# Optimization experiments

Hardware: AMD Instinct MI355X
Metric: run time of the kernel (lower is better)

The kernel has to match this reference:

```python
import jax, jax.numpy as jnp
from jax import lax
import numpy as np
import math

B, T, D = 4, 4096, 1024
K, H = 128, 8
KH = K // H
KER = 4
M = 4 * D  # mlp hidden


def _ln(x, g, b):
    m = jnp.mean(x, axis=-1, keepdims=True)
    v = jnp.var(x, axis=-1, keepdims=True)
    return (x - m) / jnp.sqrt(v + 1e-5) * g + b


def setup_inputs() -> dict:
    key = jax.random.key(0)
    ks = jax.random.split(key, 20)
    s = lambda i, shape, sc=0.02: jax.random.normal(ks[i], shape, dtype=jnp.float32) * sc
    inp = {}
    inp["x"] = jax.random.normal(ks[0], (B, T, D), dtype=jnp.float32)
    inp["prev_eig"] = jax.random.normal(ks[1], (B, T, 2 * K), dtype=jnp.float32)
    inp["in_proj_w"] = s(2, (2 * K, D))
    inp["conv_w"] = s(3, (2 * K, 1, KER), 0.3)          # depthwise Conv1d weight
    inp["conv_b"] = s(4, (2 * K,), 0.02)
    inp["mem_gate"] = jnp.float32(-3.0)
    inp["mem_proj_w"] = jnp.eye(2 * K, dtype=jnp.float32) + s(5, (2 * K, 2 * K), 0.02)
    # log_decay uniform in [center-1, center+0.5], center = -2 + 1.5*(1/5)
    center = -2.0 + 1.5 * (1.0 / 5.0)
    inp["log_decay"] = jax.random.uniform(ks[6], (K,), dtype=jnp.float32, minval=center - 1.0, maxval=center + 0.5)
    inp["frequency"] = jnp.linspace(0.0, 2.0 * math.pi * (1.0 - 1.0 / K), K, dtype=jnp.float32)
    inp["coupling"] = jnp.eye(KH, dtype=jnp.float32)[None] + 0.01 * jax.random.normal(ks[7], (H, KH, KH), dtype=jnp.float32) / math.sqrt(KH)
    inp["out_proj_w"] = s(8, (D, 2 * K))
    inp["gate_w"] = s(9, (D, D))
    inp["gate_b"] = jnp.full((D,), -2.0, dtype=jnp.float32)
    inp["mlp_w1"] = s(10, (M, D))
    inp["mlp_b1"] = jnp.zeros((M,), jnp.float32)
    inp["mlp_w2"] = s(11, (D, M))
    inp["mlp_b2"] = jnp.zeros((D,), jnp.float32)
    inp["n1_g"] = jnp.ones((D,), jnp.float32)
    inp["n1_b"] = jnp.zeros((D,), jnp.float32)
    inp["n2_g"] = jnp.ones((D,), jnp.float32)
    inp["n2_b"] = jnp.zeros((D,), jnp.float32)
    return inp


def reference(x, prev_eig, in_proj_w, conv_w, conv_b, mem_gate, mem_proj_w,
              log_decay, frequency, coupling, out_proj_w, gate_w, gate_b,
              mlp_w1, mlp_b1, mlp_w2, mlp_b2, n1_g, n1_b, n2_g, n2_b):
    Bn, Tn, Dn = x.shape
    xn = _ln(x, n1_g, n1_b)
    beta = xn @ in_proj_w.T                                   # [B,T,2K]
    # depthwise causal conv: torch pad=ker-1 both sides then [:, :, :T] == left-pad ker-1 + valid
    ker = conv_w.shape[-1]
    bp = jnp.pad(beta, ((0, 0), (ker - 1, 0), (0, 0))).transpose(0, 2, 1)  # [B,2K,T+ker-1]
    beta = lax.conv_general_dilated(bp, conv_w, (1,), 'VALID',
                                    feature_group_count=conv_w.shape[0],
                                    dimension_numbers=('NCH', 'OIH', 'NCH'))
    beta = jax.nn.silu(beta.transpose(0, 2, 1) + conv_b)       # [B,T,2K]
    br, bi = jnp.split(beta, 2, axis=-1)                       # [B,T,K] each
    # memory injection (has_memory: layer_idx > 0)
    mg = jax.nn.sigmoid(mem_gate)
    pr, pi = jnp.split(prev_eig @ mem_proj_w.T, 2, axis=-1)
    br = br + mg * pr
    bi = bi + mg * pi
    # eigenstate evolution via zero-padded complex FFT convolution
    mag = jax.nn.sigmoid(log_decay)                            # [K]
    n = jnp.arange(Tn, dtype=x.dtype)
    mag_pow = mag[None, :] ** n[:, None]                       # [T,K]
    phase = n[:, None] * frequency[None, :]
    kern = mag_pow * (jnp.cos(phase) + 1j * jnp.sin(phase))    # complex [T,K]
    beta_c = br + 1j * bi
    Bf = jnp.fft.fft(jnp.pad(beta_c, ((0, 0), (0, Tn), (0, 0))), axis=1)  # [B,2T,K]
    Kf = jnp.fft.fft(jnp.pad(kern, ((0, Tn), (0, 0))), axis=0)            # [2T,K]
    c = jnp.fft.ifft(Bf * Kf[None], axis=1)[:, :Tn]
    cr, ci = c.real.astype(x.dtype), c.imag.astype(x.dtype)
    # per-head coupling, batched over heads
    Hh, Kh = coupling.shape[0], coupling.shape[1]
    cr = jnp.einsum('hjk,bthk->bthj', coupling, cr.reshape(Bn, Tn, Hh, Kh)).reshape(Bn, Tn, Hh * Kh)
    ci = jnp.einsum('hjk,bthk->bthj', coupling, ci.reshape(Bn, Tn, Hh, Kh)).reshape(Bn, Tn, Hh * Kh)
    eig = jnp.concatenate([cr, ci], axis=-1)                   # [B,T,2K]
    h = jax.nn.sigmoid(xn @ gate_w.T + gate_b) * (eig @ out_proj_w.T)
    x1 = x + h
    y = _ln(x1, n2_g, n2_b)
    x2 = x1 + jax.nn.silu(y @ mlp_w1.T + mlp_b1) @ mlp_w2.T + mlp_b2
    return (x2, eig)
```

## Files before the change

kernel.cpp:

```cpp
#include <hip/hip_runtime.h>
#include <hip/hip_bf16.h>
#include <math.h>

#define Bn 4
#define Tn 4096
#define Dn 1024
#define Kn 128
#define TWOK 256
#define Hn 8
#define Mmlp 4096
#define NROW (Bn * Tn)
#define TAPS 16

typedef __attribute__((ext_vector_type(8))) short bf16x8;
typedef __attribute__((ext_vector_type(4))) float floatx4;

__device__ __forceinline__ float sigmoidf_(float x) { return 1.f / (1.f + __expf(-x)); }

__global__ __launch_bounds__(256) void f2bf_kernel(const float* __restrict__ in,
                                                   __hip_bfloat16* __restrict__ out,
                                                   int n) {
    const int i = (blockIdx.x * 256 + threadIdx.x) * 4;
    if (i >= n) return;
    const float4 v = *(const float4*)(in + i);
    out[i + 0] = __float2bfloat16(v.x);
    out[i + 1] = __float2bfloat16(v.y);
    out[i + 2] = __float2bfloat16(v.z);
    out[i + 3] = __float2bfloat16(v.w);
}

__global__ __launch_bounds__(256) void ln_kernel(const float* __restrict__ x,
                                                 const float* __restrict__ g,
                                                 const float* __restrict__ b,
                                                 __hip_bfloat16* __restrict__ out) {
    const int row = blockIdx.x;
    const float4* xr = (const float4*)(x + (size_t)row * Dn);
    float4 v = xr[threadIdx.x];
    float s = v.x + v.y + v.z + v.w;
    float ss = v.x * v.x + v.y * v.y + v.z * v.z + v.w * v.w;
    for (int off = 32; off; off >>= 1) {
        s += __shfl_down(s, off);
        ss += __shfl_down(ss, off);
    }
    __shared__ float rs[4], rss[4];
    const int wv = threadIdx.x >> 6, ln = threadIdx.x & 63;
    if (ln == 0) { rs[wv] = s; rss[wv] = ss; }
    __syncthreads();
    s = rs[0] + rs[1] + rs[2] + rs[3];
    ss = rss[0] + rss[1] + rss[2] + rss[3];
    const float mean = s * (1.f / Dn);
    const float var = ss * (1.f / Dn) - mean * mean;
    const float inv = rsqrtf(var + 1e-5f);
    const float4 gg = ((const float4*)g)[threadIdx.x];
    const float4 bb = ((const float4*)b)[threadIdx.x];
    __hip_bfloat16* op = out + (size_t)row * Dn + threadIdx.x * 4;
    op[0] = __float2bfloat16((v.x - mean) * inv * gg.x + bb.x);
    op[1] = __float2bfloat16((v.y - mean) * inv * gg.y + bb.y);
    op[2] = __float2bfloat16((v.z - mean) * inv * gg.z + bb.z);
    op[3] = __float2bfloat16((v.w - mean) * inv * gg.w + bb.w);
}

template <int EPI, typename CT>
__global__ __launch_bounds__(256, 4)
void gemm_bf(const ushort* __restrict__ A,
             const ushort* __restrict__ B,
             CT* __restrict__ C,
             int M, int N, int Kd,
             const float* __restrict__ bias) {
    __shared__ ushort As[128 * 32];
    __shared__ ushort Bs[128 * 32];
    const int tid = threadIdx.x;
    const int nbx = gridDim.x;
    const int nblk = nbx * gridDim.y;
    int bid = blockIdx.y * nbx + blockIdx.x;
    if ((nblk & 7) == 0)
        bid = (bid & 7) * (nblk >> 3) + (bid >> 3);
    const int m0 = (bid / nbx) * 128, n0 = (bid % nbx) * 128;
    const int wave = tid >> 6, lane = tid & 63;
    const int wm = wave >> 1, wn = wave & 1;
    const int mlane = lane & 15, quad = lane >> 4;

    floatx4 acc[4][4] = {};

    {
        const ushort* Ap = A + (size_t)m0 * Kd;
        const ushort* Bp = B + (size_t)n0 * Kd;
        for (int k0 = 0; k0 < Kd; k0 += 32) {
#pragma unroll
            for (int q = 0; q < 2; ++q) {
                const int c = q * 256 + tid;
                const int row = c >> 2, kc = (c & 3) * 8;
                __builtin_amdgcn_global_load_lds(
                    (const __attribute__((address_space(1))) void*)(Ap + (size_t)row * Kd + k0 + kc),
                    (__attribute__((address_space(3))) void*)(As + c * 8), 16, 0, 0);
                __builtin_amdgcn_global_load_lds(
                    (const __attribute__((address_space(1))) void*)(Bp + (size_t)row * Kd + k0 + kc),
                    (__attribute__((address_space(3))) void*)(Bs + c * 8), 16, 0, 0);
            }
            __syncthreads();
            bf16x8 af[4], bfr[4];
#pragma unroll
            for (int t = 0; t < 4; ++t) {
                af[t]  = *(const bf16x8*)&As[(wm * 64 + t * 16 + mlane) * 32 + quad * 8];
                bfr[t] = *(const bf16x8*)&Bs[(wn * 64 + t * 16 + mlane) * 32 + quad * 8];
            }
#pragma unroll
            for (int i = 0; i < 4; ++i)
#pragma unroll
                for (int j = 0; j < 4; ++j)
                    acc[i][j] = __builtin_amdgcn_mfma_f32_16x16x32_bf16(af[i], bfr[j], acc[i][j], 0, 0, 0);
            __syncthreads();
        }
    }

    float s_pre = 0.f;
    if constexpr (EPI == 1) s_pre = sigmoidf_(bias[0]);

    const int cbase = n0 + wn * 64 + mlane;
#pragma unroll
    for (int i = 0; i < 4; ++i) {
#pragma unroll
        for (int r = 0; r < 4; ++r) {
            const int row = m0 + wm * 64 + i * 16 + quad * 4 + r;
            const size_t ro = (size_t)row * N;
#pragma unroll
            for (int j = 0; j < 4; ++j) {
                const int col = cbase + j * 16;
                const float a = acc[i][j][r];
                float o;
                if constexpr (EPI == 0) o = a;
                else                    o = s_pre * a;
                if constexpr (__is_same(CT, float)) C[ro + col] = o;
                else                                C[ro + col] = __float2bfloat16(o);
            }
        }
    }
}

template <int EPI, typename CT>
__global__ __launch_bounds__(512, 2)
void gemmP(const ushort* __restrict__ A, const ushort* __restrict__ B,
           CT* __restrict__ C, int N, int Kd,
           const float* __restrict__ bias, const float* __restrict__ aux1,
           const __hip_bfloat16* __restrict__ aux2, int cg) {
    __shared__ ushort As[4 * 8192];
    __shared__ ushort Bs[4 * 8192];
    const int tid = threadIdx.x;
    const int nbx = gridDim.x;
    const int nblk = nbx * gridDim.y;
    const int nrows = nblk / nbx;
    int bid = blockIdx.y * nbx + blockIdx.x;
    int mt, ntile;
    if ((nblk & 7) == 0 && cg > 0 && nbx % cg == 0 && nrows % (8 / cg) == 0) {
        const int xcd = bid & 7, i = bid >> 3;
        const int cPerG = nbx / cg;
        const int rPerG = nrows / (8 / cg);
        const int rg = xcd / cg, cgi = xcd % cg;
        mt = rg * rPerG + i / cPerG;
        ntile = cgi * cPerG + i % cPerG;
    } else {
        mt = bid / nbx; ntile = bid % nbx;
    }
    const int m0 = mt * 256, n0 = ntile * 256;
    const int wave = tid >> 6, lane = tid & 63;
    const int wm = wave >> 2, wn = wave & 3;
    const int mlane = lane & 15, quad = lane >> 4;
    const int oswz = (quad ^ ((mlane >> 1) & 3)) * 8;
    const int NT = Kd >> 5;

    const int cA0 = tid, cA1 = 512 + tid;
    const int rA0 = cA0 >> 2, rA1 = cA1 >> 2;
    const ushort* aSrc0 = A + (size_t)(m0 + rA0) * Kd + (((cA0 & 3) ^ ((rA0 >> 1) & 3)) << 3);
    const ushort* aSrc1 = A + (size_t)(m0 + rA1) * Kd + (((cA1 & 3) ^ ((rA1 >> 1) & 3)) << 3);
    const ushort* bSrc0 = B + (size_t)(n0 + rA0) * Kd + (((cA0 & 3) ^ ((rA0 >> 1) & 3)) << 3);
    const ushort* bSrc1 = B + (size_t)(n0 + rA1) * Kd + (((cA1 & 3) ^ ((rA1 >> 1) & 3)) << 3);

    auto stage = [&](int t) {
        const int s = (t & 3) * 8192;
        const int kk = t << 5;
        __builtin_amdgcn_global_load_lds(
            (const __attribute__((address_space(1))) void*)(aSrc0 + kk),
            (__attribute__((address_space(3))) void*)(As + s + cA0 * 8), 16, 0, 0);
        __builtin_amdgcn_global_load_lds(
            (const __attribute__((address_space(1))) void*)(aSrc1 + kk),
            (__attribute__((address_space(3))) void*)(As + s + cA1 * 8), 16, 0, 0);
        __builtin_amdgcn_global_load_lds(
            (const __attribute__((address_space(1))) void*)(bSrc0 + kk),
            (__attribute__((address_space(3))) void*)(Bs + s + cA0 * 8), 16, 0, 0);
        __builtin_amdgcn_global_load_lds(
            (const __attribute__((address_space(1))) void*)(bSrc1 + kk),
            (__attribute__((address_space(3))) void*)(Bs + s + cA1 * 8), 16, 0, 0);
    };

    floatx4 acc[8][4] = {};
    bf16x8 fa0[8], fb0[4], fa1[8], fb1[4];

    const int arow = wm * 128 + mlane;
    const int brow = wn * 64 + mlane;

#define RDSET(FA, FB, T)                                                     \
    {                                                                        \
        const ushort* lA = As + ((T) & 3) * 8192;                            \
        const ushort* lB = Bs + ((T) & 3) * 8192;                            \
        _Pragma("unroll")                                                    \
        for (int f_ = 0; f_ < 8; ++f_)                                       \
            FA[f_] = *(const bf16x8*)(lA + (arow + f_ * 16) * 32 + oswz);    \
        _Pragma("unroll")                                                    \
        for (int g_ = 0; g_ < 4; ++g_)                                       \
            FB[g_] = *(const bf16x8*)(lB + (brow + g_ * 16) * 32 + oswz);    \
    }

#define MMSET(FA, FB)                                                        \
    __builtin_amdgcn_s_setprio(1);                                           \
    _Pragma("unroll")                                                        \
    for (int f_ = 0; f_ < 8; ++f_) {                                         \
        _Pragma("unroll")                                                    \
        for (int g_ = 0; g_ < 4; ++g_) {                                     \
            acc[f_][g_] = __builtin_amdgcn_mfma_f32_16x16x32_bf16(           \
                FA[f_], FB[g_], acc[f_][g_], 0, 0, 0);                       \
        }                                                                    \
    }                                                                        \
    __builtin_amdgcn_s_setprio(0);

#define VMW(T)                                                               \
    if ((T) + 1 < NT) { asm volatile("s_waitcnt vmcnt(4)" ::: "memory"); }   \
    else              { asm volatile("s_waitcnt vmcnt(0)" ::: "memory"); }

    stage(0); stage(1);
    VMW(0)
    __builtin_amdgcn_s_barrier();
    RDSET(fa0, fb0, 0)
    if (2 < NT) stage(2);
    VMW(1)
    __builtin_amdgcn_s_barrier();
    RDSET(fa1, fb1, 1)
    if (3 < NT) stage(3);
    MMSET(fa0, fb0)
    for (int u = 1; u < (NT >> 1); ++u) {
        const int te = 2 * u;
        VMW(te)
        __builtin_amdgcn_s_barrier();
        RDSET(fa0, fb0, te)
        if (te + 2 < NT) stage(te + 2);
        MMSET(fa1, fb1)
        const int to = te + 1;
        VMW(to)
        __builtin_amdgcn_s_barrier();
        RDSET(fa1, fb1, to)
        if (to + 2 < NT) stage(to + 2);
        MMSET(fa0, fb0)
    }
    MMSET(fa1, fb1)
#undef RDSET
#undef MMSET
#undef VMW

    const int cbase = n0 + wn * 64 + mlane;
#pragma unroll
    for (int f = 0; f < 8; ++f) {
#pragma unroll
        for (int r = 0; r < 4; ++r) {
            const int row = m0 + wm * 128 + f * 16 + quad * 4 + r;
            const size_t ro = (size_t)row * N;
#pragma unroll
            for (int g = 0; g < 4; ++g) {
                const int col = cbase + g * 16;
                const float av = acc[f][g][r];
                float o;
                if constexpr (EPI == 0) {
                    o = av;
                } else if constexpr (EPI == 2) {
                    o = aux1[ro + col] + sigmoidf_(av + bias[col]) * __bfloat162float(aux2[ro + col]);
                } else if constexpr (EPI == 3) {
                    const float tt = av + bias[col];
                    o = tt * sigmoidf_(tt);
                } else {
                    o = av + bias[col] + aux1[ro + col];
                }
                if constexpr (__is_same(CT, float)) C[ro + col] = o;
                else                                C[ro + col] = __float2bfloat16(o);
            }
        }
    }
}

#define TCH 256
#define BROWS (TCH + TAPS + 2)
#define UROWS (TCH + TAPS - 1)

__global__ __launch_bounds__(256) void cfc_kernel(const float* __restrict__ beta,
                                                  const float* __restrict__ mgp,
                                                  const float* __restrict__ conv_w,
                                                  const float* __restrict__ conv_b,
                                                  const float* __restrict__ log_decay,
                                                  const float* __restrict__ freq,
                                                  const float* __restrict__ coup,
                                                  float* __restrict__ eig,
                                                  __hip_bfloat16* __restrict__ eig_bf) {
    const int b = blockIdx.z, h = blockIdx.y, t0 = blockIdx.x * TCH;
    const int tid = threadIdx.x;

    __shared__ float sbeta[BROWS * 32];
    __shared__ float su[UROWS * 33];
    __shared__ float str[16 * TAPS], sti[16 * TAPS];
    __shared__ float scoup[16 * 16];
    __shared__ float scw[32 * 4], scb[32];

    auto chan = [&](int cg) { return (cg < 16) ? (h * 16 + cg) : (128 + h * 16 + cg - 16); };

    for (int idx = tid; idx < BROWS * 32; idx += 256) {
        const int r = idx >> 5, cg = idx & 31;
        const int t = t0 - (TAPS + 2) + r;
        sbeta[idx] = (t >= 0) ? beta[((size_t)b * Tn + t) * TWOK + chan(cg)] : 0.f;
    }
    for (int idx = tid; idx < UROWS * 32; idx += 256) {
        const int r = idx >> 5, cg = idx & 31;
        const int t = t0 - (TAPS - 1) + r;
        su[r * 33 + cg] = (t >= 0) ? mgp[((size_t)b * Tn + t) * TWOK + chan(cg)] : 0.f;
    }
    if (tid < 128) scw[tid] = conv_w[chan(tid >> 2) * 4 + (tid & 3)];
    else if (tid < 160) scb[tid - 128] = conv_b[chan(tid - 128)];
    scoup[tid] = coup[h * 256 + tid];
    {
        const int k = tid >> 4, d = tid & (TAPS - 1);
        const float mag = sigmoidf_(log_decay[h * 16 + k]);
        const float f = freq[h * 16 + k];
        const float p = powf(mag, (float)d);
        str[k * TAPS + d] = p * cosf(d * f);
        sti[k * TAPS + d] = p * sinf(d * f);
    }
    __syncthreads();

    for (int idx = tid; idx < UROWS * 32; idx += 256) {
        const int r = idx >> 5, cg = idx & 31;
        const int rb = r + 3;
        float v = sbeta[(rb - 3) * 32 + cg] * scw[cg * 4 + 0] +
                  sbeta[(rb - 2) * 32 + cg] * scw[cg * 4 + 1] +
                  sbeta[(rb - 1) * 32 + cg] * scw[cg * 4 + 2] +
                  sbeta[(rb - 0) * 32 + cg] * scw[cg * 4 + 3] + scb[cg];
        v = v * sigmoidf_(v);
        su[r * 33 + cg] += v;
    }
    __syncthreads();

    const int ru = tid + (TAPS - 1);
    float orr[16], oii[16];
#pragma unroll
    for (int j = 0; j < 16; ++j) { orr[j] = 0.f; oii[j] = 0.f; }
#pragma unroll 4
    for (int k = 0; k < 16; ++k) {
        float accr = 0.f, acci = 0.f;
#pragma unroll
        for (int d = 0; d < TAPS; ++d) {
            const float ur = su[(ru - d) * 33 + k];
            const float ui = su[(ru - d) * 33 + 16 + k];
            const float lr = str[k * TAPS + d], li = sti[k * TAPS + d];
            accr += lr * ur - li * ui;
            acci += lr * ui + li * ur;
        }
#pragma unroll
        for (int j = 0; j < 16; ++j) {
            orr[j] += scoup[j * 16 + k] * accr;
            oii[j] += scoup[j * 16 + k] * acci;
        }
    }
    const size_t base = ((size_t)b * Tn + t0 + tid) * TWOK + h * 16;
    float4* er = (float4*)(eig + base);
    float4* ei = (float4*)(eig + base + Kn);
#pragma unroll
    for (int q = 0; q < 4; ++q) {
        er[q] = make_float4(orr[4 * q], orr[4 * q + 1], orr[4 * q + 2], orr[4 * q + 3]);
        ei[q] = make_float4(oii[4 * q], oii[4 * q + 1], oii[4 * q + 2], oii[4 * q + 3]);
    }
#pragma unroll
    for (int j = 0; j < 16; ++j) {
        eig_bf[base + j] = __float2bfloat16(orr[j]);
        eig_bf[base + Kn + j] = __float2bfloat16(oii[j]);
    }
}

extern "C" void kernel_launch(void* const* d_in, const int* in_sizes, int n_in,
                              void* d_out, int out_size, void* d_ws, size_t ws_size,
                              hipStream_t stream) {
    const float* x          = (const float*)d_in[0];
    const float* prev_eig   = (const float*)d_in[1];
    const float* in_proj_w  = (const float*)d_in[2];
    const float* conv_w     = (const float*)d_in[3];
    const float* conv_b     = (const float*)d_in[4];
    const float* mem_gate   = (const float*)d_in[5];
    const float* mem_proj_w = (const float*)d_in[6];
    const float* log_decay  = (const float*)d_in[7];
    const float* frequency  = (const float*)d_in[8];
    const float* coupling   = (const float*)d_in[9];
    const float* out_proj_w = (const float*)d_in[10];
    const float* gate_w     = (const float*)d_in[11];
    const float* gate_b     = (const float*)d_in[12];
    const float* mlp_w1     = (const float*)d_in[13];
    const float* mlp_b1     = (const float*)d_in[14];
    const float* mlp_w2     = (const float*)d_in[15];
    const float* mlp_b2     = (const float*)d_in[16];
    const float* n1_g       = (const float*)d_in[17];
    const float* n1_b       = (const float*)d_in[18];
    const float* n2_g       = (const float*)d_in[19];
    const float* n2_b       = (const float*)d_in[20];

    float* out = (float*)d_out;
    float* eig = out + (size_t)NROW * Dn;

    char* wsb = (char*)d_ws;
    const size_t MB = 1 << 20;
    const bool bigws = ws_size >= 252 * MB;

    float* x1    = (float*)(wsb + 0);
    float* beta  = (float*)(wsb + 0);
    float* mgp   = (float*)(wsb + 16 * MB);
    __hip_bfloat16 *h1, *eig_bf, *peig_bf, *xn_bf, *y_bf, *w1_bf, *w2_bf,
                   *gate_bf, *inpj_bf, *outpj_bf, *mempj_bf;
    if (bigws) {
        h1       = (__hip_bfloat16*)(wsb + 64 * MB);
        xn_bf    = (__hip_bfloat16*)(wsb + 192 * MB);
        y_bf     = (__hip_bfloat16*)(wsb + 192 * MB);
        w1_bf    = (__hip_bfloat16*)(wsb + 224 * MB);
        w2_bf    = (__hip_bfloat16*)(wsb + 232 * MB);
        gate_bf  = (__hip_bfloat16*)(wsb + 240 * MB);
        inpj_bf  = (__hip_bfloat16*)(wsb + 242 * MB);
        outpj_bf = (__hip_bfloat16*)(wsb + 242 * MB + 512 * 1024);
        mempj_bf = (__hip_bfloat16*)(wsb + 243 * MB);
        peig_bf  = (__hip_bfloat16*)(wsb + 244 * MB);
        eig_bf   = (__hip_bfloat16*)(wsb + 244 * MB);
    } else {
        h1       = (__hip_bfloat16*)(wsb + 64 * MB);
        eig_bf   = (__hip_bfloat16*)(wsb + 96 * MB);
        peig_bf  = (__hip_bfloat16*)(wsb + 104 * MB);
        xn_bf    = (__hip_bfloat16*)(wsb + 128 * MB);
        y_bf     = (__hip_bfloat16*)(wsb + 160 * MB);
        w1_bf    = (__hip_bfloat16*)(wsb + 192 * MB);
        w2_bf    = (__hip_bfloat16*)(wsb + 200 * MB);
        gate_bf  = (__hip_bfloat16*)(wsb + 208 * MB);
        inpj_bf  = (__hip_bfloat16*)(wsb + 210 * MB);
        outpj_bf = (__hip_bfloat16*)(wsb + 210 * MB + 512 * 1024);
        mempj_bf = (__hip_bfloat16*)(wsb + 211 * MB);
    }

    auto cvt = [&](const float* src, __hip_bfloat16* dst, int n) {
        f2bf_kernel<<<dim3((n / 4 + 255) / 256), dim3(256), 0, stream>>>(src, dst, n);
    };
    cvt(in_proj_w,  inpj_bf,  TWOK * Dn);
    cvt(mem_proj_w, mempj_bf, TWOK * TWOK);
    cvt(out_proj_w, outpj_bf, Dn * TWOK);
    cvt(gate_w,     gate_bf,  Dn * Dn);
    cvt(mlp_w1,     w1_bf,    Mmlp * Dn);
    cvt(mlp_w2,     w2_bf,    Dn * Mmlp);
    cvt(prev_eig,   peig_bf,  NROW * TWOK);

    ln_kernel<<<dim3(NROW), dim3(256), 0, stream>>>(x, n1_g, n1_b, xn_bf);
    gemm_bf<0, float><<<dim3(2, 128), dim3(256), 0, stream>>>(
        (const ushort*)xn_bf, (const ushort*)inpj_bf, beta, NROW, TWOK, Dn, nullptr);
    gemm_bf<1, float><<<dim3(2, 128), dim3(256), 0, stream>>>(
        (const ushort*)peig_bf, (const ushort*)mempj_bf, mgp, NROW, TWOK, TWOK, mem_gate);
    cfc_kernel<<<dim3(Tn / TCH, Hn, Bn), dim3(256), 0, stream>>>(
        beta, mgp, conv_w, conv_b, log_decay, frequency, coupling, eig, eig_bf);
    gemmP<0, __hip_bfloat16><<<dim3(4, 64), dim3(512), 0, stream>>>(
        (const ushort*)eig_bf, (const ushort*)outpj_bf, h1, Dn, TWOK,
        nullptr, nullptr, nullptr, 2);
    gemmP<2, float><<<dim3(4, 64), dim3(512), 0, stream>>>(
        (const ushort*)xn_bf, (const ushort*)gate_bf, x1, Dn, Dn,
        gate_b, x, h1, 2);
    ln_kernel<<<dim3(NROW), dim3(256), 0, stream>>>(x1, n2_g, n2_b, y_bf);
    if (bigws) {
        gemmP<3, __hip_bfloat16><<<dim3(16, 64), dim3(512), 0, stream>>>(
            (const ushort*)y_bf, (const ushort*)w1_bf, h1, Mmlp, Dn,
            mlp_b1, nullptr, nullptr, 2);
        gemmP<4, float><<<dim3(4, 64), dim3(512), 0, stream>>>(
            (const ushort*)h1, (const ushort*)w2_bf, out, Dn, Mmlp,
            mlp_b2, x1, nullptr, 2);
    } else {
        for (int ck = 0; ck < 2; ++ck) {
            const size_t roff = (size_t)ck * 8192 * Dn;
            gemmP<3, __hip_bfloat16><<<dim3(16, 32), dim3(512), 0, stream>>>(
                (const ushort*)(y_bf + roff), (const ushort*)w1_bf, h1, Mmlp, Dn,
                mlp_b1, nullptr, nullptr, 2);
            gemmP<4, float><<<dim3(8, 32), dim3(512), 0, stream>>>(
                (const ushort*)h1, (const ushort*)w2_bf, out + roff, Dn, Mmlp,
                mlp_b2, x1 + roff, nullptr, 2);
        }
    }
}
```

Before: 706.4 us.

## Merge weight/input bf16 conversions into one launch and change gemmP last argument

Replaces seven separate fp32-to-bf16 conversion launches with a single grid-stride kernel that walks a concatenated index range and dispatches to the right source/destination pair. This is meant to cut launch overhead and tail effects from the small conversions. The final integer argument of several gemmP launches also changes from 2 to 1. Its meaning is not visible, but it likely selects a different scheduling or split mode for the narrow-output GEMMs.

```diff
diff --git a/kernel.cpp b/kernel.cpp
--- a/kernel.cpp
+++ b/kernel.cpp
@@ -17,16 +17,30 @@
 
 __device__ __forceinline__ float sigmoidf_(float x) { return 1.f / (1.f + __expf(-x)); }
 
-__global__ __launch_bounds__(256) void f2bf_kernel(const float* __restrict__ in,
-                                                   __hip_bfloat16* __restrict__ out,
-                                                   int n) {
-    const int i = (blockIdx.x * 256 + threadIdx.x) * 4;
-    if (i >= n) return;
-    const float4 v = *(const float4*)(in + i);
-    out[i + 0] = __float2bfloat16(v.x);
-    out[i + 1] = __float2bfloat16(v.y);
-    out[i + 2] = __float2bfloat16(v.z);
-    out[i + 3] = __float2bfloat16(v.w);
+#define MC_TOT 3555328
+__global__ __launch_bounds__(256) void multicast_kernel(
+    const float* __restrict__ s0, __hip_bfloat16* __restrict__ d0,
+    const float* __restrict__ s1, __hip_bfloat16* __restrict__ d1,
+    const float* __restrict__ s2, __hip_bfloat16* __restrict__ d2,
+    const float* __restrict__ s3, __hip_bfloat16* __restrict__ d3,
+    const float* __restrict__ s4, __hip_bfloat16* __restrict__ d4,
+    const float* __restrict__ s5, __hip_bfloat16* __restrict__ d5,
+    const float* __restrict__ s6, __hip_bfloat16* __restrict__ d6) {
+    for (int i = blockIdx.x * 256 + threadIdx.x; i < MC_TOT; i += gridDim.x * 256) {
+        const float* s; __hip_bfloat16* d; int off;
+        if      (i <   65536) { s = s0; d = d0; off = i; }
+        else if (i <   81920) { s = s1; d = d1; off = i -   65536; }
+        else if (i <  147456) { s = s2; d = d2; off = i -   81920; }
+        else if (i <  409600) { s = s3; d = d3; off = i -  147456; }
+        else if (i < 1458176) { s = s4; d = d4; off = i -  409600; }
+        else if (i < 2506752) { s = s5; d = d5; off = i - 1458176; }
+        else                  { s = s6; d = d6; off = i - 2506752; }
+        const float4 v = ((const float4*)s)[off];
+        d[off * 4 + 0] = __float2bfloat16(v.x);
+        d[off * 4 + 1] = __float2bfloat16(v.y);
+        d[off * 4 + 2] = __float2bfloat16(v.z);
+        d[off * 4 + 3] = __float2bfloat16(v.w);
+    }
 }
 
 __global__ __launch_bounds__(256) void ln_kernel(const float* __restrict__ x,
@@ -442,16 +456,14 @@
         mempj_bf = (__hip_bfloat16*)(wsb + 211 * MB);
     }
 
-    auto cvt = [&](const float* src, __hip_bfloat16* dst, int n) {
-        f2bf_kernel<<<dim3((n / 4 + 255) / 256), dim3(256), 0, stream>>>(src, dst, n);
-    };
-    cvt(in_proj_w,  inpj_bf,  TWOK * Dn);
-    cvt(mem_proj_w, mempj_bf, TWOK * TWOK);
-    cvt(out_proj_w, outpj_bf, Dn * TWOK);
-    cvt(gate_w,     gate_bf,  Dn * Dn);
-    cvt(mlp_w1,     w1_bf,    Mmlp * Dn);
-    cvt(mlp_w2,     w2_bf,    Dn * Mmlp);
-    cvt(prev_eig,   peig_bf,  NROW * TWOK);
+    multicast_kernel<<<dim3(2048), dim3(256), 0, stream>>>(
+        in_proj_w,  inpj_bf,
+        mem_proj_w, mempj_bf,
+        out_proj_w, outpj_bf,
+        gate_w,     gate_bf,
+        mlp_w1,     w1_bf,
+        mlp_w2,     w2_bf,
+        prev_eig,   peig_bf);
 
     ln_kernel<<<dim3(NROW), dim3(256), 0, stream>>>(x, n1_g, n1_b, xn_bf);
     gemm_bf<0, float><<<dim3(2, 128), dim3(256), 0, stream>>>(
@@ -462,10 +474,10 @@
         beta, mgp, conv_w, conv_b, log_decay, frequency, coupling, eig, eig_bf);
     gemmP<0, __hip_bfloat16><<<dim3(4, 64), dim3(512), 0, stream>>>(
         (const ushort*)eig_bf, (const ushort*)outpj_bf, h1, Dn, TWOK,
-        nullptr, nullptr, nullptr, 2);
+        nullptr, nullptr, nullptr, 1);
     gemmP<2, float><<<dim3(4, 64), dim3(512), 0, stream>>>(
         (const ushort*)xn_bf, (const ushort*)gate_bf, x1, Dn, Dn,
-        gate_b, x, h1, 2);
+        gate_b, x, h1, 1);
     ln_kernel<<<dim3(NROW), dim3(256), 0, stream>>>(x1, n2_g, n2_b, y_bf);
     if (bigws) {
         gemmP<3, __hip_bfloat16><<<dim3(16, 64), dim3(512), 0, stream>>>(
@@ -473,7 +485,7 @@
             mlp_b1, nullptr, nullptr, 2);
         gemmP<4, float><<<dim3(4, 64), dim3(512), 0, stream>>>(
             (const ushort*)h1, (const ushort*)w2_bf, out, Dn, Mmlp,
-            mlp_b2, x1, nullptr, 2);
+            mlp_b2, x1, nullptr, 1);
     } else {
         for (int ck = 0; ck < 2; ++ck) {
             const size_t roff = (size_t)ck * 8192 * Dn;
@@ -482,7 +494,7 @@
                 mlp_b1, nullptr, nullptr, 2);
             gemmP<4, float><<<dim3(8, 32), dim3(512), 0, stream>>>(
                 (const ushort*)h1, (const ushort*)w2_bf, out + roff, Dn, Mmlp,
-                mlp_b2, x1 + roff, nullptr, 2);
+                mlp_b2, x1 + roff, nullptr, 1);
         }
     }
 }
```

Result: faster. 658.8 us (-6.7%).
